# Optimization experiments

Measured on AMD Instinct MI355X. Metric: run time of the kernel, lower is better.

## Reference

```python
import jax, jax.numpy as jnp
import numpy as np

B, D, FH, FW, C = 8, 41, 32, 88, 64
OGFH, OGFW = 512, 1408
DX = jnp.array([0.5, 20.0, 0.5], dtype=jnp.float32)          # voxel sizes (x, y, z)
BX = jnp.array([-49.75, 0.0, -49.75], dtype=jnp.float32)    # voxel centers origin
NX = (200, 1, 200)                                           # grid dims (x, y, z)
NSEG = NX[0] * NX[1] * NX[2] * B                             # 320000 voxel-batch slots


def _frustum():
    # (D, FH, FW, 3) pixel-u, pixel-v, depth; matches create_frustum_1camera
    ds = jnp.broadcast_to(jnp.arange(4.0, 45.0, 1.0)[:, None, None], (D, FH, FW))
    xs = jnp.broadcast_to(jnp.linspace(0.0, OGFW - 1, FW)[None, None, :], (D, FH, FW))
    ys = jnp.broadcast_to(jnp.linspace(0.0, OGFH - 1, FH)[None, :, None], (D, FH, FW))
    return jnp.stack([xs, ys, ds], axis=-1).astype(jnp.float32)


def setup_inputs() -> dict:
    key = jax.random.key(0)
    k1, = jax.random.split(key, 1)
    x = jax.random.normal(k1, (B, D, FH, FW, C), dtype=jnp.float32)
    # realistic pinhole intrinsics: fx=fy=800, principal point at image center
    K = np.array([[800.0, 0.0, OGFW / 2.0],
                  [0.0, 800.0, OGFH / 2.0],
                  [0.0, 0.0, 1.0]], dtype=np.float32)
    intrins = jnp.asarray(np.broadcast_to(K, (B, 3, 3)).copy())
    post_rots = jnp.broadcast_to(jnp.eye(3, dtype=jnp.float32), (B, 3, 3)) + jnp.zeros((B, 3, 3), jnp.float32)
    post_trans = jnp.zeros((B, 3), dtype=jnp.float32)
    return {"x": x, "intrins": intrins, "post_rots": post_rots, "post_trans": post_trans}


def _forward(x, intrins, post_rots, post_trans):
    # ---- get_geometry ----
    pts = _frustum()[None] - post_trans[:, None, None, None, :]          # (B,D,FH,FW,3)
    pts = jnp.einsum('bij,bdhwj->bdhwi', jnp.linalg.inv(post_rots), pts)
    pts = jnp.concatenate([pts[..., :2] * pts[..., 2:3], pts[..., 2:3]], axis=-1)
    geom = jnp.einsum('bij,bdhwj->bdhwi', jnp.linalg.inv(intrins), pts)  # camera-frame xyz

    # ---- voxel_splat ----
    Nprime = B * D * FH * FW
    xf = x.reshape(Nprime, C)
    # torch .long() truncates toward zero -> float->int cast in jnp also truncates
    coords = ((geom - (BX - DX / 2.0)) / DX).reshape(Nprime, 3).astype(jnp.int32)
    batch_ix = jnp.repeat(jnp.arange(B, dtype=jnp.int32), Nprime // B)
    kept = ((coords[:, 0] >= 0) & (coords[:, 0] < NX[0]) &
            (coords[:, 1] >= 0) & (coords[:, 1] < NX[1]) &
            (coords[:, 2] >= 0) & (coords[:, 2] < NX[2]))
    ranks = (coords[:, 0] * (NX[1] * NX[2] * B) + coords[:, 1] * (NX[2] * B) +
             coords[:, 2] * B + batch_ix)
    ranks = jnp.where(kept, ranks, NSEG)  # dump out-of-grid points into extra segment
    # segment-sum == sort + cumsum-trick pooling (sum of features per voxel)
    pooled = jax.ops.segment_sum(xf, ranks, num_segments=NSEG + 1)[:-1]  # (NSEG, C)
    final = pooled.reshape(NX[0], NX[1], NX[2], B, C)       # rank order: (x, y, z, b)
    final = jnp.transpose(final, (3, 4, 1, 2, 0))            # (B, C, ny, nz, nx)
    # torch.cat(final.unbind(dim=2), 1) -> stack ny slices along channel dim
    out = jnp.transpose(final, (0, 2, 1, 3, 4)).reshape(B, NX[1] * C, NX[2], NX[0])
    return out


def reference(x, intrins, post_rots, post_trans):
    return _forward(x, intrins, post_rots, post_trans)
```

## Files before the change

### kernel.cpp

```cpp
#include <hip/hip_runtime.h>

#define BB 8
#define DD 41
#define FHH 32
#define FWW 88
#define CC 64
#define NXX 200
#define NXZ 200
#define PLANE (NXZ * NXX)
#define NBD (BB * DD)
#define NROWS (BB * NXZ)
#define STEPX (1407.0f / 87.0f)
#define STEPY (511.0f / 31.0f)

#define MM_OFF 0
#define CZ_OFF (NBD * FWW)
#define SLO_OFF (CZ_OFF + NBD)

__device__ __forceinline__ float invEntry(const float* __restrict__ a, int e) {
#pragma clang fp contract(off)
    float c00 = a[4] * a[8] - a[5] * a[7];
    float c01 = a[5] * a[6] - a[3] * a[8];
    float c02 = a[3] * a[7] - a[4] * a[6];
    float det = a[0] * c00 + a[1] * c01 + a[2] * c02;
    float num;
    switch (e) {
        case 0: num = c00; break;
        case 1: num = a[2] * a[7] - a[1] * a[8]; break;
        case 2: num = a[1] * a[5] - a[2] * a[4]; break;
        case 3: num = c01; break;
        case 4: num = a[0] * a[8] - a[2] * a[6]; break;
        case 5: num = a[2] * a[3] - a[0] * a[5]; break;
        case 6: num = c02; break;
        case 7: num = a[1] * a[6] - a[0] * a[7]; break;
        default: num = a[0] * a[4] - a[1] * a[3]; break;
    }
    return num / det;
}

__device__ __forceinline__ int cz_of(const float* iR, const float* iK,
                                     float t0, float t1, float t2, int d) {
#pragma clang fp contract(off)
    float dv = 4.0f + (float)d;
    float q0 = 0.0f - t0, q1 = 0.0f - t1, q2 = dv - t2;
    float p0 = fmaf(iR[2], q2, fmaf(iR[1], q1, iR[0] * q0));
    float p1 = fmaf(iR[5], q2, fmaf(iR[4], q1, iR[3] * q0));
    float p2 = fmaf(iR[8], q2, fmaf(iR[7], q1, iR[6] * q0));
    float s0 = p0 * p2, s1 = p1 * p2, s2 = p2;
    float g2 = fmaf(iK[8], s2, fmaf(iK[7], s1, iK[6] * s0));
    float czf = (g2 + 50.0f) * 2.0f;
    return (int)czf;
}

__global__ __launch_bounds__(256) void lss_meta(
        const float* __restrict__ intrins, const float* __restrict__ post_rots,
        const float* __restrict__ post_trans, int* __restrict__ wsI) {
#pragma clang fp contract(off)
    __shared__ float sInv[18];
    __shared__ unsigned smask[FWW];
    __shared__ int scx[FWW];
    int bd = blockIdx.x;
    int d = bd % DD, b = bd / DD;
    int tid = threadIdx.x;
    if (tid < 18) {
        const float* a = (tid < 9 ? post_rots : intrins) + b * 9;
        sInv[tid] = invEntry(a, tid % 9);
    }
    __syncthreads();
    const float* iR = sInv;
    const float* iK = sInv + 9;
    float t0 = post_trans[b * 3 + 0];
    float t1 = post_trans[b * 3 + 1];
    float t2 = post_trans[b * 3 + 2];
    float dv = 4.0f + (float)d;

    for (int t = tid; t < FWW * FHH; t += 256) {
        int w = t >> 5;
        int h = t & 31;
        float u = (float)w * STEPX;
        float v = (float)h * STEPY;
        float q0 = u - t0, q1 = v - t1, q2 = dv - t2;
        float p0 = fmaf(iR[2], q2, fmaf(iR[1], q1, iR[0] * q0));
        float p1 = fmaf(iR[5], q2, fmaf(iR[4], q1, iR[3] * q0));
        float p2 = fmaf(iR[8], q2, fmaf(iR[7], q1, iR[6] * q0));
        float s0 = p0 * p2, s1 = p1 * p2, s2 = p2;
        float g0 = fmaf(iK[2], s2, fmaf(iK[1], s1, iK[0] * s0));
        float g1 = fmaf(iK[5], s2, fmaf(iK[4], s1, iK[3] * s0));
        float g2 = fmaf(iK[8], s2, fmaf(iK[7], s1, iK[6] * s0));
        float cxf = (g0 + 50.0f) * 2.0f;
        float cyf = (g1 + 10.0f) / 20.0f;
        float czf = (g2 + 50.0f) * 2.0f;
        int cx = (int)cxf;
        int cy = (int)cyf;
        int cz = (int)czf;
        bool kept = (cx >= 0) & (cx < NXX) & (cy == 0) & (cz >= 0) & (cz < NXZ);
        unsigned long long m = __ballot(kept);
        int lane = tid & 63;
        int cxc = min(NXX - 1, max(0, cx));
        if (lane == 0) {
            smask[w] = (unsigned)m;
            scx[w]   = cxc;
            ((unsigned*)wsI)[MM_OFF + bd * FWW + w] = (unsigned)m;
        } else if (lane == 32) {
            smask[w] = (unsigned)(m >> 32);
            scx[w]   = cxc;
            ((unsigned*)wsI)[MM_OFF + bd * FWW + w] = (unsigned)(m >> 32);
        }
    }
    __syncthreads();
    for (int t = tid; t <= NXX; t += 256) {
        int cnt = 0;
        for (int w = 0; w < FWW; ++w) cnt += (scx[w] < t) ? 1 : 0;
        wsI[SLO_OFF + bd * (NXX + 1) + t] = cnt;
    }
    if (tid == 0)
        wsI[CZ_OFF + bd] = cz_of(iR, iK, t0, t1, t2, d);
}

__global__ __launch_bounds__(512) void lss_main(
        const float* __restrict__ x, const int* __restrict__ wsI,
        const float* __restrict__ intrins, const float* __restrict__ post_rots,
        const float* __restrict__ post_trans, float* __restrict__ out) {
#pragma clang fp contract(off)
    __shared__ float scol[FWW][CC + 1];
    __shared__ int sslo[NXX + 1];
    __shared__ unsigned ssm[FWW];
    __shared__ int sflag;
    int blk = blockIdx.x;
    int tid = threadIdx.x;

    if (blk >= NBD) {
        int r = blk - NBD;
        int b = r / NXZ, czr = r - b * NXZ;
        float* sInv = &scol[0][0];
        if (tid < 18) {
            const float* a = (tid < 9 ? post_rots : intrins) + b * 9;
            sInv[tid] = invEntry(a, tid % 9);
        }
        __syncthreads();
        if (tid < 64) {
            bool cov = false;
            if (tid < DD)
                cov = (cz_of(sInv, sInv + 9, post_trans[b * 3], post_trans[b * 3 + 1],
                             post_trans[b * 3 + 2], tid) == czr);
            unsigned long long m = __ballot(cov);
            if (tid == 0) sflag = (m != 0ull);
        }
        __syncthreads();
        if (sflag) return;
        float4 z = make_float4(0.f, 0.f, 0.f, 0.f);
        size_t base = ((size_t)b * CC) * PLANE + (size_t)czr * NXX;
        for (int i = tid; i < CC * (NXX / 4); i += 512) {
            int c = i / (NXX / 4), q = i - c * (NXX / 4);
            *reinterpret_cast<float4*>(out + base + (size_t)c * PLANE + q * 4) = z;
        }
        return;
    }

    int bd = blk;
    int b = bd / DD;
    int cz = wsI[CZ_OFF + bd];
    if (cz < 0 || cz >= NXZ) return;

    if (tid < FWW) ssm[tid] = ((const unsigned*)wsI)[MM_OFF + bd * FWW + tid];
    for (int t = tid; t <= NXX; t += 512) sslo[t] = wsI[SLO_OFF + bd * (NXX + 1) + t];
    __syncthreads();

    int wv = tid >> 6, lane = tid & 63;
    int wsub = lane >> 4, cq = lane & 15;

    for (int g = wv; g < FWW / 4; g += 8) {
        int w = g * 4 + wsub;
        unsigned m = ssm[w];
        const float* p = x + ((size_t)bd * FHH * FWW + w) * CC + (cq << 2);
        float4 acc = make_float4(0.f, 0.f, 0.f, 0.f);
#pragma unroll 4
        for (int h = 0; h < FHH; ++h) {
            float4 v = *reinterpret_cast<const float4*>(p);
            bool bt = (m >> h) & 1u;
            acc.x += bt ? v.x : 0.0f;
            acc.y += bt ? v.y : 0.0f;
            acc.z += bt ? v.z : 0.0f;
            acc.w += bt ? v.w : 0.0f;
            p += FWW * CC;
        }
        scol[w][cq * 4 + 0] = acc.x;
        scol[w][cq * 4 + 1] = acc.y;
        scol[w][cq * 4 + 2] = acc.z;
        scol[w][cq * 4 + 3] = acc.w;
    }
    __syncthreads();

    size_t base = ((size_t)b * CC) * PLANE + (size_t)cz * NXX;
    for (int j = tid; j < CC * (NXX / 4); j += 512) {
        int ch = j / (NXX / 4);
        int qq = j - ch * (NXX / 4);
        int c0 = qq * 4;
        int e0 = sslo[c0], e1 = sslo[c0 + 1], e2 = sslo[c0 + 2],
            e3 = sslo[c0 + 3], e4 = sslo[c0 + 4];
        float4 o;
        float s;
        s = 0.f; for (int w = e0; w < e1; ++w) s += scol[w][ch]; o.x = s;
        s = 0.f; for (int w = e1; w < e2; ++w) s += scol[w][ch]; o.y = s;
        s = 0.f; for (int w = e2; w < e3; ++w) s += scol[w][ch]; o.z = s;
        s = 0.f; for (int w = e3; w < e4; ++w) s += scol[w][ch]; o.w = s;
        *reinterpret_cast<float4*>(out + base + (size_t)ch * PLANE + c0) = o;
    }
}

extern "C" void kernel_launch(void* const* d_in, const int* in_sizes, int n_in,
                              void* d_out, int out_size, void* d_ws, size_t ws_size,
                              hipStream_t stream) {
    const float* x          = (const float*)d_in[0];
    const float* intrins    = (const float*)d_in[1];
    const float* post_rots  = (const float*)d_in[2];
    const float* post_trans = (const float*)d_in[3];
    float* out = (float*)d_out;
    int*   wsI = (int*)d_ws;

    lss_meta<<<NBD, 256, 0, stream>>>(intrins, post_rots, post_trans, wsI);
    lss_main<<<NBD + NROWS, 512, 0, stream>>>(x, wsI, intrins, post_rots,
                                              post_trans, out);
}
```

Measured before the change: 79.10 us.

## Fuse geometry metadata kernel into main splat kernel with shared-memory atomic row

New measurement: 73.15 us. -7.5%, faster.

```diff
diff --git a/kernel.cpp b/kernel.cpp
--- a/kernel.cpp
+++ b/kernel.cpp
@@ -10,12 +10,9 @@
 #define PLANE (NXZ * NXX)
 #define NBD (BB * DD)
 #define NROWS (BB * NXZ)
+#define ROWP 204
 #define STEPX (1407.0f / 87.0f)
 #define STEPY (511.0f / 31.0f)
-
-#define MM_OFF 0
-#define CZ_OFF (NBD * FWW)
-#define SLO_OFF (CZ_OFF + NBD)
 
 __device__ __forceinline__ float invEntry(const float* __restrict__ a, int e) {
 #pragma clang fp contract(off)
@@ -52,87 +49,24 @@
     return (int)czf;
 }
 
-__global__ __launch_bounds__(256) void lss_meta(
-        const float* __restrict__ intrins, const float* __restrict__ post_rots,
-        const float* __restrict__ post_trans, int* __restrict__ wsI) {
-#pragma clang fp contract(off)
-    __shared__ float sInv[18];
-    __shared__ unsigned smask[FWW];
-    __shared__ int scx[FWW];
-    int bd = blockIdx.x;
-    int d = bd % DD, b = bd / DD;
-    int tid = threadIdx.x;
-    if (tid < 18) {
-        const float* a = (tid < 9 ? post_rots : intrins) + b * 9;
-        sInv[tid] = invEntry(a, tid % 9);
-    }
-    __syncthreads();
-    const float* iR = sInv;
-    const float* iK = sInv + 9;
-    float t0 = post_trans[b * 3 + 0];
-    float t1 = post_trans[b * 3 + 1];
-    float t2 = post_trans[b * 3 + 2];
-    float dv = 4.0f + (float)d;
-
-    for (int t = tid; t < FWW * FHH; t += 256) {
-        int w = t >> 5;
-        int h = t & 31;
-        float u = (float)w * STEPX;
-        float v = (float)h * STEPY;
-        float q0 = u - t0, q1 = v - t1, q2 = dv - t2;
-        float p0 = fmaf(iR[2], q2, fmaf(iR[1], q1, iR[0] * q0));
-        float p1 = fmaf(iR[5], q2, fmaf(iR[4], q1, iR[3] * q0));
-        float p2 = fmaf(iR[8], q2, fmaf(iR[7], q1, iR[6] * q0));
-        float s0 = p0 * p2, s1 = p1 * p2, s2 = p2;
-        float g0 = fmaf(iK[2], s2, fmaf(iK[1], s1, iK[0] * s0));
-        float g1 = fmaf(iK[5], s2, fmaf(iK[4], s1, iK[3] * s0));
-        float g2 = fmaf(iK[8], s2, fmaf(iK[7], s1, iK[6] * s0));
-        float cxf = (g0 + 50.0f) * 2.0f;
-        float cyf = (g1 + 10.0f) / 20.0f;
-        float czf = (g2 + 50.0f) * 2.0f;
-        int cx = (int)cxf;
-        int cy = (int)cyf;
-        int cz = (int)czf;
-        bool kept = (cx >= 0) & (cx < NXX) & (cy == 0) & (cz >= 0) & (cz < NXZ);
-        unsigned long long m = __ballot(kept);
-        int lane = tid & 63;
-        int cxc = min(NXX - 1, max(0, cx));
-        if (lane == 0) {
-            smask[w] = (unsigned)m;
-            scx[w]   = cxc;
-            ((unsigned*)wsI)[MM_OFF + bd * FWW + w] = (unsigned)m;
-        } else if (lane == 32) {
-            smask[w] = (unsigned)(m >> 32);
-            scx[w]   = cxc;
-            ((unsigned*)wsI)[MM_OFF + bd * FWW + w] = (unsigned)(m >> 32);
-        }
-    }
-    __syncthreads();
-    for (int t = tid; t <= NXX; t += 256) {
-        int cnt = 0;
-        for (int w = 0; w < FWW; ++w) cnt += (scx[w] < t) ? 1 : 0;
-        wsI[SLO_OFF + bd * (NXX + 1) + t] = cnt;
-    }
-    if (tid == 0)
-        wsI[CZ_OFF + bd] = cz_of(iR, iK, t0, t1, t2, d);
-}
-
-__global__ __launch_bounds__(512) void lss_main(
-        const float* __restrict__ x, const int* __restrict__ wsI,
+__global__ __launch_bounds__(512) void lss_all(
+        const float* __restrict__ x,
         const float* __restrict__ intrins, const float* __restrict__ post_rots,
         const float* __restrict__ post_trans, float* __restrict__ out) {
 #pragma clang fp contract(off)
-    __shared__ float scol[FWW][CC + 1];
-    __shared__ int sslo[NXX + 1];
-    __shared__ unsigned ssm[FWW];
-    __shared__ int sflag;
+    __shared__ float    srow[CC * ROWP];
+    __shared__ float    sInv[18];
+    __shared__ int      scx[FWW];
+    __shared__ unsigned smask[FWW];
+    __shared__ int      scz;
+    __shared__ int      sflag;
+
     int blk = blockIdx.x;
     int tid = threadIdx.x;
 
     if (blk >= NBD) {
         int r = blk - NBD;
         int b = r / NXZ, czr = r - b * NXZ;
-        float* sInv = &scol[0][0];
         if (tid < 18) {
             const float* a = (tid < 9 ? post_rots : intrins) + b * 9;
             sInv[tid] = invEntry(a, tid % 9);
@@ -158,53 +92,105 @@
     }
 
     int bd = blk;
-    int b = bd / DD;
-    int cz = wsI[CZ_OFF + bd];
-    if (cz < 0 || cz >= NXZ) return;
-
-    if (tid < FWW) ssm[tid] = ((const unsigned*)wsI)[MM_OFF + bd * FWW + tid];
-    for (int t = tid; t <= NXX; t += 512) sslo[t] = wsI[SLO_OFF + bd * (NXX + 1) + t];
+    int d = bd % DD, b = bd / DD;
+
+    if (tid < 18) {
+        const float* a = (tid < 9 ? post_rots : intrins) + b * 9;
+        sInv[tid] = invEntry(a, tid % 9);
+    }
+    for (int i = tid; i < CC * ROWP; i += 512) srow[i] = 0.0f;
     __syncthreads();
 
-    int wv = tid >> 6, lane = tid & 63;
-    int wsub = lane >> 4, cq = lane & 15;
-
-    for (int g = wv; g < FWW / 4; g += 8) {
-        int w = g * 4 + wsub;
-        unsigned m = ssm[w];
-        const float* p = x + ((size_t)bd * FHH * FWW + w) * CC + (cq << 2);
+    {
+        const float* iR = sInv;
+        const float* iK = sInv + 9;
+        float t0 = post_trans[b * 3 + 0];
+        float t1 = post_trans[b * 3 + 1];
+        float t2 = post_trans[b * 3 + 2];
+        float dv = 4.0f + (float)d;
+        for (int t = tid; t < FWW * FHH; t += 512) {
+            int w = t >> 5;
+            int h = t & 31;
+            float u = (float)w * STEPX;
+            float v = (float)h * STEPY;
+            float q0 = u - t0, q1 = v - t1, q2 = dv - t2;
+            float p0 = fmaf(iR[2], q2, fmaf(iR[1], q1, iR[0] * q0));
+            float p1 = fmaf(iR[5], q2, fmaf(iR[4], q1, iR[3] * q0));
+            float p2 = fmaf(iR[8], q2, fmaf(iR[7], q1, iR[6] * q0));
+            float s0 = p0 * p2, s1 = p1 * p2, s2 = p2;
+            float g0 = fmaf(iK[2], s2, fmaf(iK[1], s1, iK[0] * s0));
+            float g1 = fmaf(iK[5], s2, fmaf(iK[4], s1, iK[3] * s0));
+            float g2 = fmaf(iK[8], s2, fmaf(iK[7], s1, iK[6] * s0));
+            float cxf = (g0 + 50.0f) * 2.0f;
+            float cyf = (g1 + 10.0f) / 20.0f;
+            float czf = (g2 + 50.0f) * 2.0f;
+            int cx = (int)cxf;
+            int cy = (int)cyf;
+            int cz = (int)czf;
+            bool kept = (cx >= 0) & (cx < NXX) & (cy == 0) & (cz >= 0) & (cz < NXZ);
+            unsigned long long m = __ballot(kept);
+            int lane = tid & 63;
+            int cxc = min(NXX - 1, max(0, cx));
+            if (lane == 0) {
+                smask[w] = (unsigned)m;
+                scx[w]   = cxc;
+            } else if (lane == 32) {
+                smask[w] = (unsigned)(m >> 32);
+                scx[w]   = cxc;
+            }
+            if (t == 0) scz = cz;
+        }
+    }
+    __syncthreads();
+
+    int wv   = tid >> 6;
+    int lane = tid & 63;
+    int wsub = lane >> 4;
+    int cq   = lane & 15;
+
+    for (int j = 0; j < 3; ++j) {
+        int w0 = 4 * wv + 32 * j;
+        if (w0 >= FWW) break;
+        int w = w0 + wsub;
+        unsigned m = smask[w];
+        int cx = scx[w];
+        const float* colp = x + (((size_t)bd * FHH) * FWW + w) * CC + cq * 4;
+
         float4 acc = make_float4(0.f, 0.f, 0.f, 0.f);
-#pragma unroll 4
-        for (int h = 0; h < FHH; ++h) {
-            float4 v = *reinterpret_cast<const float4*>(p);
-            bool bt = (m >> h) & 1u;
-            acc.x += bt ? v.x : 0.0f;
-            acc.y += bt ? v.y : 0.0f;
-            acc.z += bt ? v.z : 0.0f;
-            acc.w += bt ? v.w : 0.0f;
-            p += FWW * CC;
-        }
-        scol[w][cq * 4 + 0] = acc.x;
-        scol[w][cq * 4 + 1] = acc.y;
-        scol[w][cq * 4 + 2] = acc.z;
-        scol[w][cq * 4 + 3] = acc.w;
+#pragma unroll
+        for (int hb = 0; hb < 4; ++hb) {
+            if (((m >> (hb * 8)) & 0xFFu) == 0u) continue;
+            float4 vals[8];
+#pragma unroll
+            for (int k = 0; k < 8; ++k)
+                vals[k] = *reinterpret_cast<const float4*>(
+                    colp + (size_t)(hb * 8 + k) * (FWW * CC));
+#pragma unroll
+            for (int k = 0; k < 8; ++k) {
+                bool bt = (m >> (hb * 8 + k)) & 1u;
+                acc.x += bt ? vals[k].x : 0.0f;
+                acc.y += bt ? vals[k].y : 0.0f;
+                acc.z += bt ? vals[k].z : 0.0f;
+                acc.w += bt ? vals[k].w : 0.0f;
+            }
+        }
+        if (m) {
+            atomicAdd(&srow[(cq * 4 + 0) * ROWP + cx], acc.x);
+            atomicAdd(&srow[(cq * 4 + 1) * ROWP + cx], acc.y);
+            atomicAdd(&srow[(cq * 4 + 2) * ROWP + cx], acc.z);
+            atomicAdd(&srow[(cq * 4 + 3) * ROWP + cx], acc.w);
+        }
     }
     __syncthreads();
 
-    size_t base = ((size_t)b * CC) * PLANE + (size_t)cz * NXX;
-    for (int j = tid; j < CC * (NXX / 4); j += 512) {
-        int ch = j / (NXX / 4);
-        int qq = j - ch * (NXX / 4);
-        int c0 = qq * 4;
-        int e0 = sslo[c0], e1 = sslo[c0 + 1], e2 = sslo[c0 + 2],
-            e3 = sslo[c0 + 3], e4 = sslo[c0 + 4];
-        float4 o;
-        float s;
-        s = 0.f; for (int w = e0; w < e1; ++w) s += scol[w][ch]; o.x = s;
-        s = 0.f; for (int w = e1; w < e2; ++w) s += scol[w][ch]; o.y = s;
-        s = 0.f; for (int w = e2; w < e3; ++w) s += scol[w][ch]; o.z = s;
-        s = 0.f; for (int w = e3; w < e4; ++w) s += scol[w][ch]; o.w = s;
-        *reinterpret_cast<float4*>(out + base + (size_t)ch * PLANE + c0) = o;
+    int cz = scz;
+    if (cz >= 0 && cz < NXZ) {
+        size_t base = ((size_t)b * CC) * PLANE + (size_t)cz * NXX;
+        for (int i = tid; i < CC * (NXX / 4); i += 512) {
+            int c = i / (NXX / 4), q = i - c * (NXX / 4);
+            *reinterpret_cast<float4*>(out + base + (size_t)c * PLANE + q * 4) =
+                *reinterpret_cast<const float4*>(&srow[c * ROWP + q * 4]);
+        }
     }
 }
 
@@ -216,9 +202,6 @@
     const float* post_rots  = (const float*)d_in[2];
     const float* post_trans = (const float*)d_in[3];
     float* out = (float*)d_out;
-    int*   wsI = (int*)d_ws;
-
-    lss_meta<<<NBD, 256, 0, stream>>>(intrins, post_rots, post_trans, wsI);
-    lss_main<<<NBD + NROWS, 512, 0, stream>>>(x, wsI, intrins, post_rots,
-                                              post_trans, out);
-}
+
+    lss_all<<<NBD + NROWS, 512, 0, stream>>>(x, intrins, post_rots, post_trans, out);
+}
```
